# Kernel tuning notes

Hardware: AMD Instinct MI355X
Metric: run time of the kernel (lower is better)

## Reference

```python
import jax, jax.numpy as jnp
import numpy as np

NTYPES = 4
RCUT = 6.0
MIXED_TYPES = False
BOX = 40.0  # Angstrom, sets realistic atomic density


def setup_inputs() -> dict:
    key = jax.random.key(0)
    k1, k2 = jax.random.split(key)
    nframes, nloc = 2, 4096
    coord = jax.random.uniform(k1, (nframes, nloc * 3), dtype=jnp.float32) * BOX
    atype = jax.random.randint(k2, (nframes, nloc), 0, NTYPES, dtype=jnp.int32)
    return {"coord": coord, "atype": atype}


def reference(coord, atype):
    # cell=None branch: extended coords == local coords, nall == nloc
    nframes = coord.shape[0]
    c = coord.reshape(nframes, -1, 3)              # (f, nloc, 3)
    nloc = c.shape[1]
    # diff[f, i, j] = coord[j] - coord[i], shape (f, nloc, nall, 3)
    diff = c[:, None, :, :] - c[:, :, None, :]
    rr2 = jnp.sum(diff * diff, axis=-1)            # (f, nloc, nall)
    # mask self-pairs with inf (torch sets diff rows to inf before squaring)
    eye = jnp.eye(nloc, dtype=bool)
    rr2 = jnp.where(eye[None, :, :], jnp.inf, rr2)
    min_rr2 = jnp.min(rr2, axis=-1)                # (f, nloc)
    mask = rr2 < RCUT ** 2                         # (f, nloc, nall)
    if not MIXED_TYPES:
        # per-type neighbor counts via one-hot contraction (replaces the
        # Python loop over ntypes in the torch code; same math)
        onehot = jax.nn.one_hot(atype, NTYPES, dtype=jnp.int32)  # (f, nall, t)
        nnei = jnp.einsum('fij,fjt->fit', mask.astype(jnp.int32), onehot)
    else:
        valid = (atype >= 0)[:, None, :]
        nnei = jnp.sum(mask & valid, axis=-1).astype(jnp.int32)[..., None]
    max_nnei = jnp.max(nnei, axis=1)               # (f, ntypes) or (f, 1)
    return min_rr2, max_nnei
```

## Files before the change

### kernel.cpp

```cpp
#include <hip/hip_runtime.h>
#include <stdint.h>

#define NFRAMES 2
#define NT 4
#define BLK 256
#define NJ 64

template <bool SELFCHK>
__device__ __forceinline__ void do_pair(const float* __restrict__ cf,
                                        const int* __restrict__ tf,
                                        int j, int i,
                                        float xi, float yi, float zi,
                                        float& mm, unsigned& cc) {
#pragma clang fp contract(off)
    float dx = cf[3 * j]     - xi;
    float dy = cf[3 * j + 1] - yi;
    float dz = cf[3 * j + 2] - zi;
    unsigned sval = 1u << (tf[j] * 8);
    float xx = dx * dx;
    float yy = dy * dy;
    float zz = dz * dz;
    float r2 = (xx + yy) + zz;
    bool self = SELFCHK && (j == i);
    float rm = self ? __builtin_inff() : r2;
    mm = fminf(mm, rm);
    bool near = (r2 < 36.0f) && !self;
    cc += near ? sval : 0u;
}

__global__ __launch_bounds__(BLK) void ns_pair_kernel(const float* __restrict__ coord,
                                                      const int* __restrict__ atype,
                                                      uint2* __restrict__ part,
                                                      int nloc) {
    const int f = blockIdx.z;
    const int ibase = blockIdx.y * BLK;
    const int i = ibase + threadIdx.x;
    const int jslice = nloc / NJ;
    const int jb = blockIdx.x;
    const int jbase = jb * jslice;

    const float* cf = coord + (size_t)f * nloc * 3;
    const int*   tf = atype + (size_t)f * nloc;

    const float xi = cf[3 * i];
    const float yi = cf[3 * i + 1];
    const float zi = cf[3 * i + 2];

    float m0 = __builtin_inff(), m1 = __builtin_inff();
    unsigned c0 = 0u, c1 = 0u;

    const bool overlap = (jbase >= ibase) && (jbase < ibase + BLK);

    if (overlap) {
#pragma unroll 8
        for (int j = jbase; j < jbase + jslice; j += 2) {
            do_pair<true>(cf, tf, j,     i, xi, yi, zi, m0, c0);
            do_pair<true>(cf, tf, j + 1, i, xi, yi, zi, m1, c1);
        }
    } else {
#pragma unroll 8
        for (int j = jbase; j < jbase + jslice; j += 2) {
            do_pair<false>(cf, tf, j,     i, xi, yi, zi, m0, c0);
            do_pair<false>(cf, tf, j + 1, i, xi, yi, zi, m1, c1);
        }
    }

    float minr2 = fminf(m0, m1);
    unsigned c = c0 + c1;

    part[((size_t)jb * NFRAMES + f) * nloc + i] =
        make_uint2(__float_as_uint(minr2), c);
}

__global__ __launch_bounds__(BLK) void ns_finalize_kernel(const uint2* __restrict__ part,
                                                          float* __restrict__ out,
                                                          int* __restrict__ pmax,
                                                          int nloc) {
    const int nbpf = nloc / BLK;
    const int f  = blockIdx.x / nbpf;
    const int ib = blockIdx.x % nbpf;
    const int i  = ib * BLK + threadIdx.x;

    float m = __builtin_inff();
    unsigned c = 0u;
#pragma unroll 16
    for (int jb = 0; jb < NJ; ++jb) {
        uint2 v = part[((size_t)jb * NFRAMES + f) * nloc + i];
        m = fminf(m, __uint_as_float(v.x));
        c += v.y;
    }
    out[(size_t)f * nloc + i] = m;

    int m0 = (int)(c & 255u);
    int m1 = (int)((c >> 8) & 255u);
    int m2 = (int)((c >> 16) & 255u);
    int m3 = (int)(c >> 24);
    for (int off = 32; off > 0; off >>= 1) {
        m0 = max(m0, __shfl_xor(m0, off, 64));
        m1 = max(m1, __shfl_xor(m1, off, 64));
        m2 = max(m2, __shfl_xor(m2, off, 64));
        m3 = max(m3, __shfl_xor(m3, off, 64));
    }
    __shared__ int red[BLK / 64][NT];
    int wid = threadIdx.x >> 6;
    if ((threadIdx.x & 63) == 0) {
        red[wid][0] = m0; red[wid][1] = m1; red[wid][2] = m2; red[wid][3] = m3;
    }
    __syncthreads();
    if (threadIdx.x < NT) {
        int t = threadIdx.x;
        pmax[blockIdx.x * NT + t] =
            max(max(red[0][t], red[1][t]), max(red[2][t], red[3][t]));
    }
}

__global__ __launch_bounds__(64) void ns_max_kernel(const int* __restrict__ pmax,
                                                    float* __restrict__ out,
                                                    int nbpf, int nloc) {
    const int t = threadIdx.x;
    if (t < NFRAMES * NT) {
        const int f = t / NT, tt = t % NT;
        int m = 0;
        for (int b = 0; b < nbpf; ++b)
            m = max(m, pmax[(f * nbpf + b) * NT + tt]);
        out[(size_t)NFRAMES * nloc + f * NT + tt] = (float)m;
    }
}

extern "C" void kernel_launch(void* const* d_in, const int* in_sizes, int n_in,
                              void* d_out, int out_size, void* d_ws, size_t ws_size,
                              hipStream_t stream) {
    const float* coord = (const float*)d_in[0];
    const int*   atype = (const int*)d_in[1];
    const int nloc = in_sizes[1] / NFRAMES;

    float* out = (float*)d_out;
    uint2* part = (uint2*)d_ws;
    int*   pmax = (int*)((char*)d_ws + (size_t)NJ * NFRAMES * nloc * sizeof(uint2));

    dim3 grid(NJ, nloc / BLK, NFRAMES);
    ns_pair_kernel<<<grid, dim3(BLK), 0, stream>>>(coord, atype, part, nloc);

    const int nbpf = nloc / BLK;
    ns_finalize_kernel<<<NFRAMES * nbpf, BLK, 0, stream>>>(part, out, pmax, nloc);

    ns_max_kernel<<<1, 64, 0, stream>>>(pmax, out, nbpf, nloc);
}
```

Before: 27.51 us.

## Process two i-atoms per thread to reuse j coordinate loads, double j-slices

New measurement: 27.28 us. No clear change (-0.9%).

```diff
diff --git a/kernel.cpp b/kernel.cpp
--- a/kernel.cpp
+++ b/kernel.cpp
@@ -4,19 +4,17 @@
 #define NFRAMES 2
 #define NT 4
 #define BLK 256
-#define NJ 64
+#define NJ 128
 
 template <bool SELFCHK>
-__device__ __forceinline__ void do_pair(const float* __restrict__ cf,
-                                        const int* __restrict__ tf,
+__device__ __forceinline__ void do_pair(float cx, float cy, float cz, unsigned sval,
                                         int j, int i,
                                         float xi, float yi, float zi,
                                         float& mm, unsigned& cc) {
 #pragma clang fp contract(off)
-    float dx = cf[3 * j]     - xi;
-    float dy = cf[3 * j + 1] - yi;
-    float dz = cf[3 * j + 2] - zi;
-    unsigned sval = 1u << (tf[j] * 8);
+    float dx = cx - xi;
+    float dy = cy - yi;
+    float dz = cz - zi;
     float xx = dx * dx;
     float yy = dy * dy;
     float zz = dz * dz;
@@ -33,8 +31,11 @@
                                                       uint2* __restrict__ part,
                                                       int nloc) {
     const int f = blockIdx.z;
-    const int ibase = blockIdx.y * BLK;
-    const int i = ibase + threadIdx.x;
+    const int half = nloc >> 1;
+    const int ibase1 = blockIdx.y * BLK;
+    const int ibase2 = ibase1 + half;
+    const int i1 = ibase1 + threadIdx.x;
+    const int i2 = ibase2 + threadIdx.x;
     const int jslice = nloc / NJ;
     const int jb = blockIdx.x;
     const int jbase = jb * jslice;
@@ -42,34 +43,45 @@
     const float* cf = coord + (size_t)f * nloc * 3;
     const int*   tf = atype + (size_t)f * nloc;
 
-    const float xi = cf[3 * i];
-    const float yi = cf[3 * i + 1];
-    const float zi = cf[3 * i + 2];
+    const float x1 = cf[3 * i1], y1 = cf[3 * i1 + 1], z1 = cf[3 * i1 + 2];
+    const float x2 = cf[3 * i2], y2 = cf[3 * i2 + 1], z2 = cf[3 * i2 + 2];
 
-    float m0 = __builtin_inff(), m1 = __builtin_inff();
-    unsigned c0 = 0u, c1 = 0u;
+    float m1a = __builtin_inff(), m1b = __builtin_inff();
+    float m2a = __builtin_inff(), m2b = __builtin_inff();
+    unsigned c1a = 0u, c1b = 0u, c2a = 0u, c2b = 0u;
 
-    const bool overlap = (jbase >= ibase) && (jbase < ibase + BLK);
+    const bool overlap = (jbase >= ibase1 && jbase < ibase1 + BLK) ||
+                         (jbase >= ibase2 && jbase < ibase2 + BLK);
 
     if (overlap) {
-#pragma unroll 8
+#pragma unroll 4
         for (int j = jbase; j < jbase + jslice; j += 2) {
-            do_pair<true>(cf, tf, j,     i, xi, yi, zi, m0, c0);
-            do_pair<true>(cf, tf, j + 1, i, xi, yi, zi, m1, c1);
+            float cx0 = cf[3 * j],     cy0 = cf[3 * j + 1], cz0 = cf[3 * j + 2];
+            unsigned s0 = 1u << (tf[j] * 8);
+            do_pair<true>(cx0, cy0, cz0, s0, j, i1, x1, y1, z1, m1a, c1a);
+            do_pair<true>(cx0, cy0, cz0, s0, j, i2, x2, y2, z2, m2a, c2a);
+            float cx1 = cf[3 * j + 3], cy1 = cf[3 * j + 4], cz1 = cf[3 * j + 5];
+            unsigned s1 = 1u << (tf[j + 1] * 8);
+            do_pair<true>(cx1, cy1, cz1, s1, j + 1, i1, x1, y1, z1, m1b, c1b);
+            do_pair<true>(cx1, cy1, cz1, s1, j + 1, i2, x2, y2, z2, m2b, c2b);
         }
     } else {
-#pragma unroll 8
+#pragma unroll 4
         for (int j = jbase; j < jbase + jslice; j += 2) {
-            do_pair<false>(cf, tf, j,     i, xi, yi, zi, m0, c0);
-            do_pair<false>(cf, tf, j + 1, i, xi, yi, zi, m1, c1);
+            float cx0 = cf[3 * j],     cy0 = cf[3 * j + 1], cz0 = cf[3 * j + 2];
+            unsigned s0 = 1u << (tf[j] * 8);
+            do_pair<false>(cx0, cy0, cz0, s0, j, i1, x1, y1, z1, m1a, c1a);
+            do_pair<false>(cx0, cy0, cz0, s0, j, i2, x2, y2, z2, m2a, c2a);
+            float cx1 = cf[3 * j + 3], cy1 = cf[3 * j + 4], cz1 = cf[3 * j + 5];
+            unsigned s1 = 1u << (tf[j + 1] * 8);
+            do_pair<false>(cx1, cy1, cz1, s1, j + 1, i1, x1, y1, z1, m1b, c1b);
+            do_pair<false>(cx1, cy1, cz1, s1, j + 1, i2, x2, y2, z2, m2b, c2b);
         }
     }
 
-    float minr2 = fminf(m0, m1);
-    unsigned c = c0 + c1;
-
-    part[((size_t)jb * NFRAMES + f) * nloc + i] =
-        make_uint2(__float_as_uint(minr2), c);
+    const size_t base = ((size_t)jb * NFRAMES + f) * nloc;
+    part[base + i1] = make_uint2(__float_as_uint(fminf(m1a, m1b)), c1a + c1b);
+    part[base + i2] = make_uint2(__float_as_uint(fminf(m2a, m2b)), c2a + c2b);
 }
 
 __global__ __launch_bounds__(BLK) void ns_finalize_kernel(const uint2* __restrict__ part,
@@ -81,15 +93,19 @@
     const int ib = blockIdx.x % nbpf;
     const int i  = ib * BLK + threadIdx.x;
 
-    float m = __builtin_inff();
-    unsigned c = 0u;
-#pragma unroll 16
-    for (int jb = 0; jb < NJ; ++jb) {
-        uint2 v = part[((size_t)jb * NFRAMES + f) * nloc + i];
-        m = fminf(m, __uint_as_float(v.x));
-        c += v.y;
+    float ma = __builtin_inff(), mb = __builtin_inff();
+    unsigned ca = 0u, cb = 0u;
+#pragma unroll 8
+    for (int jb = 0; jb < NJ; jb += 2) {
+        uint2 va = part[((size_t)jb * NFRAMES + f) * nloc + i];
+        uint2 vb = part[((size_t)(jb + 1) * NFRAMES + f) * nloc + i];
+        ma = fminf(ma, __uint_as_float(va.x));
+        mb = fminf(mb, __uint_as_float(vb.x));
+        ca += va.y;
+        cb += vb.y;
     }
-    out[(size_t)f * nloc + i] = m;
+    out[(size_t)f * nloc + i] = fminf(ma, mb);
+    unsigned c = ca + cb;
 
     int m0 = (int)(c & 255u);
     int m1 = (int)((c >> 8) & 255u);
@@ -138,7 +154,7 @@
     uint2* part = (uint2*)d_ws;
     int*   pmax = (int*)((char*)d_ws + (size_t)NJ * NFRAMES * nloc * sizeof(uint2));
 
-    dim3 grid(NJ, nloc / BLK, NFRAMES);
+    dim3 grid(NJ, nloc / (BLK * 2), NFRAMES);
     ns_pair_kernel<<<grid, dim3(BLK), 0, stream>>>(coord, atype, part, nloc);
 
     const int nbpf = nloc / BLK;
```
